# Optimization experiments

Hardware: AMD Instinct MI355X
Metric: run time of the kernel (lower is better)

The kernel has to match this reference:

```python
import jax, jax.numpy as jnp
import numpy as np

N_NODES = 100000
N_EDGES = 1600000
D_IN, D_HID, D_OUT = 256, 128, 64


def setup_inputs() -> dict:
    key = jax.random.key(0)
    k = jax.random.split(key, 6)
    x = jax.random.normal(k[0], (N_NODES, D_IN), dtype=jnp.float32)
    edge_index = jax.random.randint(k[1], (2, N_EDGES), 0, N_NODES, dtype=jnp.int64)
    W1 = jax.random.normal(k[2], (D_IN, D_HID), dtype=jnp.float32) / np.sqrt(D_IN)
    b1 = jnp.zeros((D_HID,), dtype=jnp.float32)
    W2 = jax.random.normal(k[3], (D_HID, D_OUT), dtype=jnp.float32) / np.sqrt(D_HID)
    b2 = jnp.zeros((D_OUT,), dtype=jnp.float32)
    return {"x": x, "edge_index": edge_index, "W1": W1, "b1": b1, "W2": W2, "b2": b2}


def gcn_conv(x, W, b, src, dst, n):
    """PyG GCNConv: h = D^-1/2 (A+I) D^-1/2 (x W) + b, symmetric norm with self-loops."""
    h = x @ W                                           # [n, d_out]
    # degree from destination (col) index, +1 for the self-loop edge weight
    deg = jnp.ones((n,), x.dtype).at[dst].add(jnp.float32(1.0))
    dinv = jax.lax.rsqrt(deg)                           # deg >= 1, no inf
    norm = dinv[src] * dinv[dst]                        # [E]
    agg = jax.ops.segment_sum(h[src] * norm[:, None], dst, num_segments=n)
    agg = agg + h * (dinv * dinv)[:, None]              # self-loop contribution
    return agg + b


def reference(x, edge_index, W1, b1, W2, b2):
    src, dst = edge_index[0], edge_index[1]
    n = x.shape[0]
    h = gcn_conv(x, W1, b1, src, dst, n)
    h = jax.nn.relu(h)                                  # dropout is identity in eval mode
    out = gcn_conv(h, W2, b2, src, dst, n)
    return out
```

## Files before the change

### kernel.cpp

```cpp
#include <hip/hip_runtime.h>
#include <stdint.h>

typedef unsigned short u16;
typedef unsigned int u32;
typedef __bf16 bf16x8 __attribute__((ext_vector_type(8)));
typedef float floatx4 __attribute__((ext_vector_type(4)));

static __device__ __forceinline__ float bf2f(u16 u) {
  union { u32 i; float f; } v; v.i = ((u32)u) << 16; return v.f;
}
static __device__ __forceinline__ u16 f2bf(float f) {
  union { float f; u32 i; } v; v.f = f;
  u32 u = v.i;
  return (u16)((u + 0x7fffu + ((u >> 16) & 1u)) >> 16);
}

static __device__ __forceinline__ void gload_lds16_nt(const void* g, void* l) {
  __builtin_amdgcn_global_load_lds(
      (const __attribute__((address_space(1))) void*)g,
      (__attribute__((address_space(3))) void*)l, 16, 0, 2);
}

static __device__ __forceinline__ int edge_m64(const int* ei, int lane) {
  return (__ballot(ei[2 * lane + 1] == 0) == ~0ull) ? 1 : 0;
}

static __device__ __forceinline__ int edge_src(const int* ei, int E, int i, int m64) {
  return m64 ? ei[2 * (size_t)i] : ei[i];
}
static __device__ __forceinline__ int edge_dst(const int* ei, int E, int i, int m64) {
  return m64 ? ei[2 * (size_t)E + 2 * (size_t)i] : ei[(size_t)E + i];
}

__global__ void k_transpose(const float* __restrict__ W1, const float* __restrict__ W2,
                            u16* __restrict__ Wt1, u16* __restrict__ Wt2) {
  int i = blockIdx.x * 256 + threadIdx.x;
  if (i < 256 * 128) {
    int k = i >> 7, c = i & 127;
    Wt1[c * 256 + k] = f2bf(W1[i]);
  } else {
    int j = i - 256 * 128;
    if (j < 128 * 64) {
      int k = j >> 6, c = j & 63;
      Wt2[c * 128 + k] = f2bf(W2[j]);
    }
  }
}

#define CHUNK 2048

__global__ void k_count(const int* __restrict__ ei, int E,
                        int* __restrict__ bucket_cnt, int NB) {
  __shared__ int h[1024];
  const int t = threadIdx.x;
  const int m64 = edge_m64(ei, t & 63);
  for (int i = t; i < 1024; i += 256) h[i] = 0;
  __syncthreads();
  const int c0 = blockIdx.x * CHUNK;
  const int cnt = min(CHUNK, E - c0);
  for (int i = t; i < cnt; i += 256)
    atomicAdd(&h[edge_dst(ei, E, c0 + i, m64) >> 7], 1);
  __syncthreads();
  for (int i = t; i < NB; i += 256)
    if (h[i]) atomicAdd(&bucket_cnt[i], h[i]);
}

__global__ void k_bscan(const int* __restrict__ bucket_cnt, int* __restrict__ bucket_base,
                        int* __restrict__ bucket_cursor, int NB,
                        int* __restrict__ row_ptr, int n, int E) {
  __shared__ int ts[256];
  const int t = threadIdx.x;
  const int b4 = t * 4;
  int a0 = (b4 + 0 < NB) ? bucket_cnt[b4 + 0] : 0;
  int a1 = (b4 + 1 < NB) ? bucket_cnt[b4 + 1] : 0;
  int a2 = (b4 + 2 < NB) ? bucket_cnt[b4 + 2] : 0;
  int a3 = (b4 + 3 < NB) ? bucket_cnt[b4 + 3] : 0;
  int p1 = a0, p2 = p1 + a1, p3 = p2 + a2, tsum = p3 + a3;
  ts[t] = tsum;
  __syncthreads();
  for (int off = 1; off < 256; off <<= 1) {
    int x = (t >= off) ? ts[t - off] : 0;
    __syncthreads();
    ts[t] += x;
    __syncthreads();
  }
  int ex0 = ts[t] - tsum;
  int e[4] = {ex0, ex0 + p1, ex0 + p2, ex0 + p3};
#pragma unroll
  for (int j = 0; j < 4; ++j) {
    int i = b4 + j;
    if (i < NB) { bucket_base[i] = e[j]; bucket_cursor[i] = e[j]; }
  }
  if (t == 0) row_ptr[n] = E + n;
}

__global__ void k_place(const int* __restrict__ ei, int E,
                        int* __restrict__ bucket_cursor, uint2* __restrict__ pairs, int NB) {
  __shared__ int h[1024];
  __shared__ int ex[1024];
  __shared__ int cur[1024];
  __shared__ int ts[256];
  __shared__ uint2 stage[CHUNK];
  const int t = threadIdx.x;
  const int c0 = blockIdx.x * CHUNK;
  const int cnt = min(CHUNK, E - c0);
  const int m64 = edge_m64(ei, t & 63);

  for (int i = t; i < 1024; i += 256) h[i] = 0;
  __syncthreads();

  int es[8], ed[8];
#pragma unroll
  for (int j = 0; j < 8; ++j) {
    int i = t + j * 256;
    es[j] = 0; ed[j] = -1;
    if (i < cnt) {
      es[j] = edge_src(ei, E, c0 + i, m64);
      ed[j] = edge_dst(ei, E, c0 + i, m64);
      atomicAdd(&h[ed[j] >> 7], 1);
    }
  }
  __syncthreads();

  const int b4 = t * 4;
  int a0 = h[b4], a1 = h[b4 + 1], a2 = h[b4 + 2], a3 = h[b4 + 3];
  int p1 = a0, p2 = p1 + a1, p3 = p2 + a2, tsum = p3 + a3;
  ts[t] = tsum;
  __syncthreads();
  for (int off = 1; off < 256; off <<= 1) {
    int x = (t >= off) ? ts[t - off] : 0;
    __syncthreads();
    ts[t] += x;
    __syncthreads();
  }
  int ex0 = ts[t] - tsum;
  ex[b4] = ex0;       cur[b4] = ex0;
  ex[b4 + 1] = ex0 + p1; cur[b4 + 1] = ex0 + p1;
  ex[b4 + 2] = ex0 + p2; cur[b4 + 2] = ex0 + p2;
  ex[b4 + 3] = ex0 + p3; cur[b4 + 3] = ex0 + p3;
  __syncthreads();

#pragma unroll
  for (int j = 0; j < 8; ++j) {
    if (ed[j] >= 0) {
      int b = ed[j] >> 7;
      int pos = atomicAdd(&cur[b], 1);
      stage[pos] = make_uint2((u32)es[j], (u32)ed[j]);
    }
  }
  __syncthreads();
  for (int i = t; i < NB; i += 256) {
    int c = h[i];
    if (c > 0) h[i] = atomicAdd(&bucket_cursor[i], c);
  }
  __syncthreads();

  for (int i = t; i < cnt; i += 256) {
    uint2 p = stage[i];
    int b = (int)(p.y >> 7);
    pairs[h[b] + (i - ex[b])] = p;
  }
}

#define BMAX 3072
__global__ void k_csr(const uint2* __restrict__ pairs, const int* __restrict__ bucket_cnt,
                      const int* __restrict__ bucket_base, int* __restrict__ row_ptr,
                      float* __restrict__ dinv, int* __restrict__ srcs, int n) {
  __shared__ int h[128], cur[128];
  __shared__ int lsrc[BMAX];
  const int b = blockIdx.x;
  const int t = threadIdx.x;
  const int cnt = bucket_cnt[b];
  const int base = bucket_base[b];
  const int nbase = base + b * 128;

  if (t < 128) h[t] = 0;
  __syncthreads();
  for (int i = t; i < cnt; i += 256)
    atomicAdd(&h[pairs[base + i].y & 127], 1);
  __syncthreads();

  __shared__ int sc[128];
  int v = 0;
  if (t < 128) { v = h[t]; sc[t] = v; }
  __syncthreads();
  for (int off = 1; off < 128; off <<= 1) {
    int x = 0;
    if (t < 128 && t >= off) x = sc[t - off];
    __syncthreads();
    if (t < 128) sc[t] += x;
    __syncthreads();
  }
  if (t < 128) {
    int excl = sc[t] - v;
    cur[t] = excl + t + 1;
    int node = b * 128 + t;
    if (node < n) {
      row_ptr[node] = nbase + excl + t;
      dinv[node] = rsqrtf(1.0f + (float)v);
      int sp = excl + t;
      if (sp < BMAX) lsrc[sp] = node;
      else srcs[nbase + sp] = node;
    }
  }
  __syncthreads();

  for (int i = t; i < cnt; i += 256) {
    uint2 p = pairs[base + i];
    int pos = atomicAdd(&cur[p.y & 127], 1);
    if (pos < BMAX) lsrc[pos] = (int)p.x;
    else srcs[nbase + pos] = (int)p.x;
  }
  __syncthreads();
  const int lim = min(cnt + 128, BMAX);
  for (int i = t; i < lim; i += 256) srcs[nbase + i] = lsrc[i];
}

template<int N, int K, int CHK, bool A_FP32>
__launch_bounds__(256, 4)
__global__ void k_gemm(const void* __restrict__ Ap, const u16* __restrict__ Wt,
                       const float* __restrict__ dinv, u16* __restrict__ G, int M)
{
  constexpr int ESZ  = A_FP32 ? 4 : 2;
  constexpr int BPR  = K * ESZ;
  constexpr int BPRC = CHK * ESZ;
  constexpr int RPI  = 1024 / BPRC;
  constexpr int NISS = 64 / RPI;
  constexpr int STRIDE = 1024 + 16;
  constexpr int NCH  = K / CHK;
  constexpr int KSC  = CHK / 32;
  constexpr int IPW  = NISS / 4;
  constexpr int LPR  = BPRC / 16;
  constexpr int SWM  = 8 / RPI;
  constexpr int NT   = N / 32;
  __shared__ char lds[2 * NISS * STRIDE];
  const int t = threadIdx.x;
  const int wave = t >> 6, lane = t & 63;
  const int row0 = blockIdx.x * 64;
  const int wr = wave >> 1, wc = wave & 1;
  const int lm = lane & 15, lq = lane >> 4;

  const int ril  = lane / LPR;
  const int scol = ((lane % LPR) ^ (ril * SWM)) * 16;

  auto stage = [&](int kc) {
    char* buf = lds + (size_t)(kc & 1) * (NISS * STRIDE);
    const size_t kb = (size_t)kc * BPRC;
#pragma unroll
    for (int i = 0; i < IPW; ++i) {
      const int g = wave * IPW + i;
      int r0 = row0 + g * RPI;
      if (r0 < M) {
        if (r0 > M - RPI) r0 = M - RPI;
        gload_lds16_nt((const char*)Ap + (size_t)(r0 + ril) * BPR + kb + scol,
                       buf + g * STRIDE);
      }
    }
  };

  floatx4 acc[2][NT];
#pragma unroll
  for (int i = 0; i < 2; ++i)
#pragma unroll
    for (int j = 0; j < NT; ++j) acc[i][j] = (floatx4)(0.0f);

  const int arow = wr * 32 + lm;
  const u16* pb = Wt + (size_t)(wc * (N / 2) + lm) * K + lq * 8;

  stage(0);

#pragma unroll
  for (int c = 0; c < NCH; ++c) {
    bf16x8 breg[KSC][NT];
#pragma unroll
    for (int ksl = 0; ksl < KSC; ++ksl)
#pragma unroll
      for (int nt = 0; nt < NT; ++nt)
        breg[ksl][nt] = *(const bf16x8*)(pb + (size_t)nt * 16 * K + (c * KSC + ksl) * 32);

    if (c + 1 < NCH) {
      stage(c + 1);
      asm volatile("s_waitcnt vmcnt(%0)" :: "i"(IPW) : "memory");
    } else {
      asm volatile("s_waitcnt vmcnt(0)" ::: "memory");
    }
    __builtin_amdgcn_sched_barrier(0);
    __builtin_amdgcn_s_barrier();
    __builtin_amdgcn_sched_barrier(0);

    const char* buf = lds + (size_t)(c & 1) * (NISS * STRIDE);
#pragma unroll
    for (int ksl = 0; ksl < KSC; ++ksl) {
      bf16x8 a[2];
#pragma unroll
      for (int mt = 0; mt < 2; ++mt) {
        const int r = arow + mt * 16;
        const int cb = (ksl * 32 + lq * 8) * ESZ;
        const char* p = buf + (r / RPI) * STRIDE + (r % RPI) * BPRC
                        + (cb ^ ((r % RPI) * SWM * 16));
        if constexpr (A_FP32) {
          float4 f0 = *(const float4*)p;
          float4 f1 = *(const float4*)(p + 16);
          bf16x8 av;
          av[0] = (__bf16)f0.x; av[1] = (__bf16)f0.y; av[2] = (__bf16)f0.z; av[3] = (__bf16)f0.w;
          av[4] = (__bf16)f1.x; av[5] = (__bf16)f1.y; av[6] = (__bf16)f1.z; av[7] = (__bf16)f1.w;
          a[mt] = av;
        } else {
          a[mt] = *(const bf16x8*)p;
        }
      }
#pragma unroll
      for (int nt = 0; nt < NT; ++nt) {
        acc[0][nt] = __builtin_amdgcn_mfma_f32_16x16x32_bf16(a[0], breg[ksl][nt], acc[0][nt], 0, 0, 0);
        acc[1][nt] = __builtin_amdgcn_mfma_f32_16x16x32_bf16(a[1], breg[ksl][nt], acc[1][nt], 0, 0, 0);
      }
    }
    __builtin_amdgcn_sched_barrier(0);
    __builtin_amdgcn_s_barrier();
  }

  const int crow0 = row0 + wr * 32 + lq * 4;
#pragma unroll
  for (int mt = 0; mt < 2; ++mt) {
#pragma unroll
    for (int nt = 0; nt < NT; ++nt) {
      const int gc = wc * (N / 2) + nt * 16 + lm;
#pragma unroll
      for (int r = 0; r < 4; ++r) {
        const int gr = crow0 + mt * 16 + r;
        if (gr < M) G[(size_t)gr * N + gc] = f2bf(acc[mt][nt][r] * dinv[gr]);
      }
    }
  }
}

template<int F, bool RELU, bool OUT_BF16, int NPW>
__launch_bounds__(256, 8)
__global__ void k_agg(const u16* __restrict__ g, const int* __restrict__ row_ptr,
                      const int* __restrict__ srcs, const float* __restrict__ dinv,
                      const float* __restrict__ bias, void* __restrict__ outp, int n)
{
  const int wid = blockIdx.x * 4 + (threadIdx.x >> 6);
  const int n0 = wid * NPW;
  if (n0 >= n) return;
  const int n1 = min(n0 + NPW, n);
  const int lane = threadIdx.x & 63;
  constexpr int VPL = F / 64;
  const int col = lane * VPL;
  const float b0 = bias[col];
  const float b1 = (VPL == 2) ? bias[col + (VPL - 1)] : 0.f;

  int e    = __builtin_amdgcn_readfirstlane(row_ptr[n0]);
  int eEnd = __builtin_amdgcn_readfirstlane(row_ptr[n1]);
  int cur  = n0;
  int nb   = __builtin_amdgcn_readfirstlane(row_ptr[n0 + 1]);
  float dv = dinv[n0];
  float a0 = 0.f, a1 = 0.f;

  auto fin = [&]() {
    float o0 = dv * a0 + b0;
    if (RELU) o0 = fmaxf(o0, 0.f);
    if constexpr (VPL == 2) {
      float o1 = dv * a1 + b1;
      if (RELU) o1 = fmaxf(o1, 0.f);
      if constexpr (OUT_BF16) {
        u32 pk = (u32)f2bf(o0) | ((u32)f2bf(o1) << 16);
        *(u32*)((u16*)outp + (size_t)cur * F + col) = pk;
      } else {
        *(float2*)((float*)outp + (size_t)cur * F + col) = make_float2(o0, o1);
      }
    } else {
      if constexpr (OUT_BF16) ((u16*)outp)[(size_t)cur * F + col] = f2bf(o0);
      else                    ((float*)outp)[(size_t)cur * F + col] = o0;
    }
    ++cur;
    a0 = 0.f; a1 = 0.f;
    if (cur < n) {
      dv = dinv[cur];
      nb = __builtin_amdgcn_readfirstlane(row_ptr[cur + 1]);
    }
  };

  auto issue = [&](int eb, u32* gv) {
    const int* sp = srcs + eb;
#pragma unroll
    for (int j = 0; j < 8; ++j) {
      const int s = sp[j];
      if constexpr (VPL == 2)
        gv[j] = *(const u32*)(g + (size_t)s * F + col);
      else
        gv[j] = (u32)g[(size_t)s * F + col];
    }
  };

  auto consume = [&](int eb, const u32* gv) {
#pragma unroll
    for (int j = 0; j < 8; ++j) {
      if (eb + j == nb) fin();
      if constexpr (VPL == 2) {
        a0 += bf2f((u16)gv[j]);
        a1 += bf2f((u16)(gv[j] >> 16));
      } else {
        a0 += bf2f((u16)gv[j]);
      }
    }
  };

  u32 gvA[8], gvB[8];
  const int rem = (eEnd - e) >> 3;
  if (rem >= 1) issue(e, gvA);
  if (rem >= 2) issue(e + 8, gvB);
  int i = 0;
  for (; i + 2 < rem; i += 2) {
    consume(e + i * 8, gvA);
    issue(e + (i + 2) * 8, gvA);
    consume(e + (i + 1) * 8, gvB);
    if (i + 3 < rem) issue(e + (i + 3) * 8, gvB);
  }
  if (i < rem) { consume(e + i * 8, gvA); ++i; }
  if (i < rem) { consume(e + i * 8, gvB); ++i; }

  for (int et = e + rem * 8; et < eEnd; ++et) {
    const int s = srcs[et];
    u32 gvt;
    if constexpr (VPL == 2) gvt = *(const u32*)(g + (size_t)s * F + col);
    else                    gvt = (u32)g[(size_t)s * F + col];
    if (et == nb) fin();
    if constexpr (VPL == 2) { a0 += bf2f((u16)gvt); a1 += bf2f((u16)(gvt >> 16)); }
    else                    a0 += bf2f((u16)gvt);
  }
  fin();
}

extern "C" void kernel_launch(void* const* d_in, const int* in_sizes, int n_in,
                              void* d_out, int out_size, void* d_ws, size_t ws_size,
                              hipStream_t stream)
{
  const float* x  = (const float*)d_in[0];
  const int*   ei = (const int*)d_in[1];
  const float* W1 = (const float*)d_in[2];
  const float* b1 = (const float*)d_in[3];
  const float* W2 = (const float*)d_in[4];
  const float* b2 = (const float*)d_in[5];

  const int n = in_sizes[0] / 256;
  const int E = in_sizes[1] / 2;
  const int NB = (n + 127) >> 7;

  char* ws = (char*)d_ws;
  size_t off = 0;
  auto alloc = [&](size_t bytes) -> void* {
    void* p = ws + off;
    off = (off + bytes + 255) & ~(size_t)255;
    return p;
  };
  int*   row_ptr = (int*)alloc((size_t)(n + 1) * 4);
  int*   bcnt    = (int*)alloc(1024 * 4);
  int*   bbase   = (int*)alloc(1024 * 4);
  int*   bcur    = (int*)alloc(1024 * 4);
  float* dinv    = (float*)alloc((size_t)n * 4);
  u16*   Wt1     = (u16*)alloc(256 * 128 * 2);
  u16*   Wt2     = (u16*)alloc(128 * 64 * 2);
  uint2* pairs   = (uint2*)alloc((size_t)E * 8);
  int*   srcs    = (int*)alloc((size_t)(E + n + 512) * 4);
  u16*   g1      = (u16*)alloc((size_t)n * 128 * 2);
  u16*   y1      = (u16*)alloc((size_t)n * 128 * 2);
  u16*   g2      = (u16*)alloc((size_t)n * 64 * 2);
  (void)ws_size; (void)n_in; (void)out_size;

  const int TB = 256;
  const int nbC = (E + CHUNK - 1) / CHUNK;

  hipMemsetAsync(bcnt, 0, 1024 * 4, stream);
  k_transpose<<<(256 * 128 + 128 * 64 + TB - 1) / TB, TB, 0, stream>>>(W1, W2, Wt1, Wt2);
  k_count<<<nbC, TB, 0, stream>>>(ei, E, bcnt, NB);
  k_bscan<<<1, TB, 0, stream>>>(bcnt, bbase, bcur, NB, row_ptr, n, E);
  k_place<<<nbC, TB, 0, stream>>>(ei, E, bcur, pairs, NB);
  k_csr<<<NB, TB, 0, stream>>>(pairs, bcnt, bbase, row_ptr, dinv, srcs, n);

  constexpr int NPW = 8;
  const int nwaves = (n + NPW - 1) / NPW;
  const int aggGrid = (nwaves + 3) / 4;

  k_gemm<128, 256, 64, true><<<(n + 63) / 64, 256, 0, stream>>>(x, Wt1, dinv, g1, n);
  k_agg<128, true, true, NPW><<<aggGrid, 256, 0, stream>>>(g1, row_ptr, srcs, dinv, b1, y1, n);
  k_gemm<64, 128, 64, false><<<(n + 63) / 64, 256, 0, stream>>>(y1, Wt2, dinv, g2, n);
  k_agg<64, false, false, NPW><<<aggGrid, 256, 0, stream>>>(g2, row_ptr, srcs, dinv, b2, d_out, n);
}
```

Baseline: 372.0 us.

## Split each wavefront into two half-waves gathering different edges per aggregation step

The aggregation kernel now has each 32-lane half of a wavefront gather a different neighbor row, using wider per-lane loads (8 or 4 bytes instead of 4 or 2). The two halves' partial sums are combined with a cross-half shuffle at each node boundary. This halves the number of load instructions per edge and gives each lane a wider memory access, aiming to raise gather throughput. In exchange it adds shuffle and select overhead, plus branchy handling of node boundaries that fall inside an edge pair.

```diff
diff --git a/kernel.cpp b/kernel.cpp
--- a/kernel.cpp
+++ b/kernel.cpp
@@ -334,79 +334,118 @@
   }
 }
 
+template<int ACC> struct gsel;
+template<> struct gsel<4> { using T = uint2; };
+template<> struct gsel<2> { using T = u32; };
+
 template<int F, bool RELU, bool OUT_BF16, int NPW>
 __launch_bounds__(256, 8)
 __global__ void k_agg(const u16* __restrict__ g, const int* __restrict__ row_ptr,
                       const int* __restrict__ srcs, const float* __restrict__ dinv,
                       const float* __restrict__ bias, void* __restrict__ outp, int n)
 {
+  constexpr int ACC = F / 32;
+  using gvt = typename gsel<ACC>::T;
   const int wid = blockIdx.x * 4 + (threadIdx.x >> 6);
   const int n0 = wid * NPW;
   if (n0 >= n) return;
   const int n1 = min(n0 + NPW, n);
   const int lane = threadIdx.x & 63;
-  constexpr int VPL = F / 64;
-  const int col = lane * VPL;
-  const float b0 = bias[col];
-  const float b1 = (VPL == 2) ? bias[col + (VPL - 1)] : 0.f;
+  const int half = lane >> 5;
+  const int sub = lane & 31;
+  const int col = sub * ACC;
+
+  float bs[ACC];
+#pragma unroll
+  for (int j = 0; j < ACC; ++j) bs[j] = bias[col + j];
 
   int e    = __builtin_amdgcn_readfirstlane(row_ptr[n0]);
   int eEnd = __builtin_amdgcn_readfirstlane(row_ptr[n1]);
   int cur  = n0;
   int nb   = __builtin_amdgcn_readfirstlane(row_ptr[n0 + 1]);
   float dv = dinv[n0];
-  float a0 = 0.f, a1 = 0.f;
+  float a[ACC];
+#pragma unroll
+  for (int j = 0; j < ACC; ++j) a[j] = 0.f;
+
+  auto unpack = [&](gvt v, float* o) {
+    if constexpr (ACC == 4) {
+      o[0] = bf2f((u16)v.x); o[1] = bf2f((u16)(v.x >> 16));
+      o[2] = bf2f((u16)v.y); o[3] = bf2f((u16)(v.y >> 16));
+    } else {
+      o[0] = bf2f((u16)v); o[1] = bf2f((u16)(v >> 16));
+    }
+  };
 
   auto fin = [&]() {
-    float o0 = dv * a0 + b0;
-    if (RELU) o0 = fmaxf(o0, 0.f);
-    if constexpr (VPL == 2) {
-      float o1 = dv * a1 + b1;
-      if (RELU) o1 = fmaxf(o1, 0.f);
+    float o[ACC];
+#pragma unroll
+    for (int j = 0; j < ACC; ++j) {
+      float tot = a[j] + __shfl_xor(a[j], 32);
+      o[j] = dv * tot + bs[j];
+      if (RELU) o[j] = fmaxf(o[j], 0.f);
+      a[j] = 0.f;
+    }
+    if (lane < 32) {
       if constexpr (OUT_BF16) {
-        u32 pk = (u32)f2bf(o0) | ((u32)f2bf(o1) << 16);
-        *(u32*)((u16*)outp + (size_t)cur * F + col) = pk;
+        u16* out = (u16*)outp + (size_t)cur * F + col;
+        if constexpr (ACC == 4) {
+          u32 p0 = (u32)f2bf(o[0]) | ((u32)f2bf(o[1]) << 16);
+          u32 p1 = (u32)f2bf(o[2]) | ((u32)f2bf(o[3]) << 16);
+          *(uint2*)out = make_uint2(p0, p1);
+        } else {
+          *(u32*)out = (u32)f2bf(o[0]) | ((u32)f2bf(o[1]) << 16);
+        }
       } else {
-        *(float2*)((float*)outp + (size_t)cur * F + col) = make_float2(o0, o1);
+        float* out = (float*)outp + (size_t)cur * F + col;
+        if constexpr (ACC == 4) *(float4*)out = make_float4(o[0], o[1], o[2], o[3]);
+        else                    *(float2*)out = make_float2(o[0], o[1]);
       }
-    } else {
-      if constexpr (OUT_BF16) ((u16*)outp)[(size_t)cur * F + col] = f2bf(o0);
-      else                    ((float*)outp)[(size_t)cur * F + col] = o0;
     }
     ++cur;
-    a0 = 0.f; a1 = 0.f;
     if (cur < n) {
       dv = dinv[cur];
       nb = __builtin_amdgcn_readfirstlane(row_ptr[cur + 1]);
     }
   };
 
-  auto issue = [&](int eb, u32* gv) {
+  auto addAll = [&](gvt v) {
+    float u[ACC]; unpack(v, u);
+#pragma unroll
+    for (int j = 0; j < ACC; ++j) a[j] += u[j];
+  };
+  auto addHalf = [&](gvt v, int h) {
+    float u[ACC]; unpack(v, u);
+#pragma unroll
+    for (int j = 0; j < ACC; ++j) a[j] += (half == h) ? u[j] : 0.f;
+  };
+
+  auto issue = [&](int eb, gvt* gv) {
     const int* sp = srcs + eb;
 #pragma unroll
-    for (int j = 0; j < 8; ++j) {
-      const int s = sp[j];
-      if constexpr (VPL == 2)
-        gv[j] = *(const u32*)(g + (size_t)s * F + col);
-      else
-        gv[j] = (u32)g[(size_t)s * F + col];
-    }
-  };
-
-  auto consume = [&](int eb, const u32* gv) {
-#pragma unroll
-    for (int j = 0; j < 8; ++j) {
-      if (eb + j == nb) fin();
-      if constexpr (VPL == 2) {
-        a0 += bf2f((u16)gv[j]);
-        a1 += bf2f((u16)(gv[j] >> 16));
+    for (int i = 0; i < 4; ++i) {
+      const int sa = sp[2 * i], sb = sp[2 * i + 1];
+      const int s = half ? sb : sa;
+      gv[i] = *(const gvt*)(g + (size_t)s * F + col);
+    }
+  };
+
+  auto consume = [&](int eb, const gvt* gv) {
+#pragma unroll
+    for (int i = 0; i < 4; ++i) {
+      const int e0 = eb + 2 * i, e1 = e0 + 1;
+      if (nb <= e1) {
+        if (nb == e0) fin();
+        addHalf(gv[i], 0);
+        if (nb == e1) fin();
+        addHalf(gv[i], 1);
       } else {
-        a0 += bf2f((u16)gv[j]);
+        addAll(gv[i]);
       }
     }
   };
 
-  u32 gvA[8], gvB[8];
+  gvt gvA[4], gvB[4];
   const int rem = (eEnd - e) >> 3;
   if (rem >= 1) issue(e, gvA);
   if (rem >= 2) issue(e + 8, gvB);
@@ -422,12 +461,9 @@
 
   for (int et = e + rem * 8; et < eEnd; ++et) {
     const int s = srcs[et];
-    u32 gvt;
-    if constexpr (VPL == 2) gvt = *(const u32*)(g + (size_t)s * F + col);
-    else                    gvt = (u32)g[(size_t)s * F + col];
+    gvt v = *(const gvt*)(g + (size_t)s * F + col);
     if (et == nb) fin();
-    if constexpr (VPL == 2) { a0 += bf2f((u16)gvt); a1 += bf2f((u16)(gvt >> 16)); }
-    else                    a0 += bf2f((u16)gvt);
+    addHalf(v, 0);
   }
   fin();
 }
```

Result: no change. 366.2 us (-1.6%).
